# Kernel tuning notes

Measured on AMD Instinct MI355X. Metric: run time of the kernel, lower is better.

## Reference

```python
import jax, jax.numpy as jnp
import numpy as np

K_DEPTH = 3
JAC_A = 1.0  # alpha (Jacobi a)
JAC_B = 1.0  # beta  (Jacobi b)


def jacobi_filter(sig, gammas):
    """Polynomial graph filter g(sigma) = sum_k gamma_k * P_k^{(a,b)}(sigma),
    Jacobi recurrence applied elementwise (Sigma is diagonal spectrum), domain [-1,1],
    fixed inner scalings (fixI=True => alphas=1)."""
    a, b = JAC_A, JAC_B
    xs = [jnp.ones_like(sig)]
    # L = 1
    coef1 = (a - b) / 2.0
    coef2 = (a + b + 2.0) / 2.0
    xs.append(coef1 * xs[0] + coef2 * sig * xs[0])
    for L in range(2, K_DEPTH + 1):
        cl = 2.0 * L * (L + a + b) * (2 * L - 2 + a + b)
        c1 = (2 * L + a + b - 1) * (2 * L + a + b) * (2 * L + a + b - 2)
        c2 = (2 * L + a + b - 1) * (a * a - b * b)
        c3 = 2.0 * (L - 1 + a) * (L - 1 + b) * (2 * L + a + b)
        xs.append((c1 / cl) * sig * xs[-1] - (c2 / cl) * xs[-1] - (c3 / cl) * xs[-2])
    basis = jnp.stack(xs, axis=0)  # [K+1, B, H, L, d]
    return jnp.einsum('k,kbhld->bhld', gammas, basis)


def setup_inputs() -> dict:
    key = jax.random.key(0)
    ks = jax.random.split(key, 7)
    B, L, Ha, Hs, d = 4, 2048, 4, 4, 64
    mk = lambda k, H: jax.random.normal(k, (B, L, H, d), dtype=jnp.float32)
    return {
        'U': mk(ks[0], Ha),
        'Sigma': mk(ks[1], Ha),
        'V': mk(ks[2], Ha),
        'values': mk(ks[3], Ha),
        'queries_softmax': mk(ks[4], Hs),
        'keys_softmax': mk(ks[5], Hs),
        'values_softmax': mk(ks[6], Hs),
        'gammas': jnp.ones((K_DEPTH + 1,), dtype=jnp.float32),
    }


def reference(U, Sigma, V, values, queries_softmax, keys_softmax, values_softmax, gammas):
    d_k = U.shape[-1]
    # ---- AGF (SVD) heads ----
    Uh = jax.nn.softmax(jnp.transpose(U, (0, 2, 1, 3)), axis=-1)        # [B,H,L,d]
    Vt = jax.nn.softmax(jnp.transpose(V, (0, 2, 3, 1)), axis=-1)        # [B,H,d,L]
    vals = jnp.transpose(values, (0, 2, 1, 3))                           # [B,H,L,d]
    sig = jax.nn.sigmoid(jnp.transpose(Sigma, (0, 2, 1, 3)))             # [B,H,L,d]
    gf = jacobi_filter(sig, gammas)                                       # [B,H,L,d]
    kv = jnp.einsum('bhdl,bhle->bhde', Vt, vals)                          # [B,H,d,d]
    out_agf = jnp.einsum('bhld,bhde->bhle', Uh * gf, kv)                  # [B,H,L,d]
    out_agf = jnp.transpose(out_agf, (0, 2, 1, 3))                        # [B,L,H,d]
    # ---- orthogonality loss ----
    eye = jnp.eye(d_k, dtype=Uh.dtype)
    sym_u = jnp.einsum('bhld,bhle->bhde', Uh, Uh) - eye
    sym_v = jnp.einsum('bhdl,bhel->bhde', Vt, Vt) - eye
    ortho_loss = jnp.mean(jnp.abs(sym_u), axis=(1, 2, 3)) + jnp.mean(jnp.abs(sym_v), axis=(1, 2, 3))
    # ---- softmax (flash) heads ----
    q = jnp.transpose(queries_softmax, (0, 2, 1, 3))
    k = jnp.transpose(keys_softmax, (0, 2, 1, 3))
    v = jnp.transpose(values_softmax, (0, 2, 1, 3))
    scores = jnp.einsum('bhld,bhsd->bhls', q, k) / jnp.sqrt(jnp.asarray(d_k, q.dtype))
    attn = jax.nn.softmax(scores, axis=-1)
    out_sm = jnp.einsum('bhls,bhsd->bhld', attn, v)
    out_sm = jnp.transpose(out_sm, (0, 2, 1, 3))                          # [B,L,H,d]
    out = jnp.concatenate([out_agf, out_sm], axis=2)                      # [B,L,2H,d]
    return out, ortho_loss
```

## Files before the change

kernel.cpp:

```cpp
#include <hip/hip_runtime.h>
#include <hip/hip_bf16.h>

#define BB 4
#define SEQ 2048
#define NH 4
#define D 64
#define NPAIR 16
#define HOUT 8
#define LOSS_BASE ((size_t)BB * SEQ * HOUT * D)

#define N_PART   (4 * 16 * 3 * 4096)
#define OFF_SPART N_PART
#define N_SPART  (16 * 32 * 64)
#define OFF_LPART (OFF_SPART + N_SPART)
#define N_LPART  (2 * 16 * 2048)
#define OFF_F32_END (OFF_LPART + N_LPART)
#define USZ ((size_t)16 * 2048 * 64)

typedef __attribute__((ext_vector_type(8))) short bf16x8;
typedef __attribute__((ext_vector_type(4))) float f32x4;
typedef __attribute__((ext_vector_type(8))) unsigned short us8;
typedef __attribute__((ext_vector_type(4))) unsigned short us4;

__device__ __forceinline__ unsigned short f2bf(float x) {
    union { float f; unsigned u; } v; v.f = x;
    unsigned r = v.u + 0x7fffu + ((v.u >> 16) & 1u);
    return (unsigned short)(r >> 16);
}
__device__ __forceinline__ float bf2f(unsigned short u) {
    union { unsigned u; float f; } v; v.u = ((unsigned)u) << 16; return v.f;
}
__device__ __forceinline__ void load16(const float* p, float* v) {
    const float4* q = (const float4*)p;
    float4 a = q[0], b = q[1], c = q[2], d = q[3];
    v[0]=a.x; v[1]=a.y; v[2]=a.z; v[3]=a.w;
    v[4]=b.x; v[5]=b.y; v[6]=b.z; v[7]=b.w;
    v[8]=c.x; v[9]=c.y; v[10]=c.z; v[11]=c.w;
    v[12]=d.x; v[13]=d.y; v[14]=d.z; v[15]=d.w;
}
__device__ __forceinline__ void wr_bf16x16(unsigned short* dst, const float* v) {
    us8 w0, w1;
#pragma unroll
    for (int i = 0; i < 8; i++) { w0[i] = f2bf(v[i]); w1[i] = f2bf(v[8 + i]); }
    *(us8*)dst = w0; *(us8*)(dst + 8) = w1;
}

__global__ __launch_bounds__(256) void prep(const float* __restrict__ U, const float* __restrict__ Sg,
                                            const float* __restrict__ Vagf, const float* __restrict__ vals,
                                            const float* __restrict__ Ksm, const float* __restrict__ Vsm,
                                            const float* __restrict__ gam,
                                            float* __restrict__ ws, unsigned short* __restrict__ usb,
                                            float* __restrict__ out) {
    int lt = blockIdx.x, p = blockIdx.y, stage = blockIdx.z;
    int b = p >> 2, h = p & 3;
    int tid = threadIdx.x;
    int r = tid >> 2;
    int c0 = (tid & 3) * 16;
    __shared__ float T[64][68];
    unsigned short* Khi   = usb;
    unsigned short* VbfT  = usb + USZ;
    unsigned short* UhT   = usb + 2 * USZ;
    unsigned short* EhiT  = usb + 3 * USZ;
    unsigned short* valsT = usb + 4 * USZ;
    unsigned short* Ughi  = usb + 5 * USZ;
    unsigned short* Uglo  = usb + 6 * USZ;
    float* Spart = ws + OFF_SPART;

    const size_t gbase = ((size_t)(b * SEQ + lt * 64 + r) * NH + h) * D + c0;
    const size_t nbase = ((size_t)(p * SEQ + lt * 64 + r)) * 64 + c0;
    const size_t tbase = ((size_t)p * 64 + r) * 2048 + lt * 64 + c0;
    float v[16], e[16];

    if (stage == 0) {
        load16(U + gbase, v);
        float mx = v[0];
#pragma unroll
        for (int k = 1; k < 16; k++) mx = fmaxf(mx, v[k]);
        mx = fmaxf(mx, __shfl_xor(mx, 1));
        mx = fmaxf(mx, __shfl_xor(mx, 2));
        float sm = 0.0f;
#pragma unroll
        for (int k = 0; k < 16; k++) { v[k] = __expf(v[k] - mx); sm += v[k]; }
        sm += __shfl_xor(sm, 1);
        sm += __shfl_xor(sm, 2);
        float inv = 1.0f / sm;
#pragma unroll
        for (int k = 0; k < 16; k++) { v[k] *= inv; T[r][c0 + k] = v[k]; }
        float sg[16];
        load16(Sg + gbase, sg);
        float g0 = gam[0], g1 = gam[1], g2 = gam[2], g3 = gam[3];
        us8 h0, h1, l0, l1;
#pragma unroll
        for (int k = 0; k < 16; k++) {
            float sig = 1.0f / (1.0f + __expf(-sg[k]));
            float x1 = 2.0f * sig;
            float x2 = 1.875f * sig * x1 - 0.75f;
            float x3 = 1.8666666666666667f * sig * x2 - 0.8f * x1;
            float ug = v[k] * (g0 + g1 * x1 + g2 * x2 + g3 * x3);
            unsigned short hh = f2bf(ug);
            unsigned short ll = f2bf(ug - bf2f(hh));
            if (k < 8) { h0[k] = hh; l0[k] = ll; } else { h1[k - 8] = hh; l1[k - 8] = ll; }
        }
        *(us8*)(Ughi + nbase) = h0; *(us8*)(Ughi + nbase + 8) = h1;
        *(us8*)(Uglo + nbase) = l0; *(us8*)(Uglo + nbase + 8) = l1;
        __syncthreads();
#pragma unroll
        for (int k = 0; k < 16; k++) e[k] = T[c0 + k][r];
        wr_bf16x16(UhT + tbase, e);
    } else if (stage == 1) {
        load16(Vagf + gbase, v);
#pragma unroll
        for (int k = 0; k < 16; k++) T[r][c0 + k] = __expf(v[k]);
        __syncthreads();
        float ssum = 0.0f;
#pragma unroll
        for (int k = 0; k < 16; k++) { e[k] = T[c0 + k][r]; ssum += e[k]; }
        ssum += __shfl_xor(ssum, 1);
        ssum += __shfl_xor(ssum, 2);
        if ((tid & 3) == 0) Spart[(p * 32 + lt) * 64 + r] = ssum;
        wr_bf16x16(EhiT + tbase, e);
    } else if (stage == 2) {
        load16(vals + gbase, v);
#pragma unroll
        for (int k = 0; k < 16; k++) T[r][c0 + k] = v[k];
        __syncthreads();
#pragma unroll
        for (int k = 0; k < 16; k++) e[k] = T[c0 + k][r];
        wr_bf16x16(valsT + tbase, e);
    } else if (stage == 3) {
        load16(Vsm + gbase, v);
#pragma unroll
        for (int k = 0; k < 16; k++) T[r][c0 + k] = v[k];
        __syncthreads();
#pragma unroll
        for (int k = 0; k < 16; k++) e[k] = T[c0 + k][r];
        wr_bf16x16(VbfT + tbase, e);
    } else {
        load16(Ksm + gbase, v);
        wr_bf16x16(Khi + nbase, v);
        if (lt == 0 && p == 0 && tid < BB) out[LOSS_BASE + tid] = 0.0f;
    }
}

#define PSTR 72

__global__ __launch_bounds__(256, 2) void mid(const unsigned short* __restrict__ usb,
                                              const float* __restrict__ Q,
                                              float* __restrict__ part,
                                              unsigned short* __restrict__ OpartUS,
                                              float* __restrict__ lpart) {
    __shared__ __align__(16) unsigned char smem[36864];
    const int bid = blockIdx.x;
    const int tid = threadIdx.x;
    const int w = tid >> 6, lane = tid & 63, lm = lane & 15, quad = lane >> 4;

    if (bid >= 64) {
        int fb = bid - 64;
        int qt2 = fb & 15, p = (fb >> 4) & 15, half = fb >> 8;
        int b = p >> 2, h = p & 3;
        const unsigned short* Khi  = usb;
        const unsigned short* VbfT = usb + USZ;
        unsigned short* Kl = (unsigned short*)smem;
        unsigned short* Vl = Kl + 64 * PSTR;
        unsigned short* Ph = Vl + 64 * PSTR;
        const int srow = tid >> 2, sseg = (tid & 3) * 16;

        bf16x8 qhi[2][2], qlo[2][2];
#pragma unroll
        for (int q = 0; q < 2; q++) {
            int row = qt2 * 128 + q * 64 + w * 16 + lm;
            const float* qp = Q + ((size_t)(b * SEQ + row) * NH + h) * D + quad * 8;
#pragma unroll
            for (int ks = 0; ks < 2; ks++) {
                float qq[8];
                float4 a0 = *(const float4*)(qp + ks * 32);
                float4 a1 = *(const float4*)(qp + ks * 32 + 4);
                qq[0]=a0.x; qq[1]=a0.y; qq[2]=a0.z; qq[3]=a0.w;
                qq[4]=a1.x; qq[5]=a1.y; qq[6]=a1.z; qq[7]=a1.w;
#pragma unroll
                for (int j = 0; j < 8; j++) {
                    float xs = qq[j] * 0.125f;
                    unsigned short hi = f2bf(xs);
                    qhi[q][ks][j] = (short)hi;
                    qlo[q][ks][j] = (short)f2bf(xs - bf2f(hi));
                }
            }
        }

        float rsum[2] = {0.f, 0.f};
        f32x4 o[2][4];
#pragma unroll
        for (int q = 0; q < 2; q++)
#pragma unroll
            for (int t = 0; t < 4; t++) o[q][t] = (f32x4){0.f, 0.f, 0.f, 0.f};

        for (int kt = 0; kt < 16; ++kt) {
            __syncthreads();
            {
                size_t kb = ((size_t)(p * SEQ + half * 1024 + kt * 64 + srow)) * 64 + sseg;
                us8 k0 = *(const us8*)(Khi + kb);
                us8 k1 = *(const us8*)(Khi + kb + 8);
                size_t vb = ((size_t)p * 64 + srow) * 2048 + half * 1024 + kt * 64 + sseg;
                us8 v0 = *(const us8*)(VbfT + vb);
                us8 v1 = *(const us8*)(VbfT + vb + 8);
                *(us8*)&Kl[srow * PSTR + sseg] = k0; *(us8*)&Kl[srow * PSTR + sseg + 8] = k1;
                *(us8*)&Vl[srow * PSTR + sseg] = v0; *(us8*)&Vl[srow * PSTR + sseg + 8] = v1;
            }
            __syncthreads();

            bf16x8 kfr[4][2], vfr[4][2];
#pragma unroll
            for (int t = 0; t < 4; t++)
#pragma unroll
                for (int ks = 0; ks < 2; ks++) {
                    kfr[t][ks] = *(const bf16x8*)&Kl[(t * 16 + lm) * PSTR + ks * 32 + quad * 8];
                    vfr[t][ks] = *(const bf16x8*)&Vl[(t * 16 + lm) * PSTR + ks * 32 + quad * 8];
                }

#pragma unroll
            for (int q = 0; q < 2; q++) {
                unsigned short* Phq = Ph + (size_t)(w * 2 + q) * 16 * PSTR;
                f32x4 s[4];
#pragma unroll
                for (int t = 0; t < 4; t++) s[t] = (f32x4){0.f, 0.f, 0.f, 0.f};
#pragma unroll
                for (int t = 0; t < 4; t++)
#pragma unroll
                    for (int ks = 0; ks < 2; ks++) {
                        s[t] = __builtin_amdgcn_mfma_f32_16x16x32_bf16(kfr[t][ks], qhi[q][ks], s[t], 0, 0, 0);
                        s[t] = __builtin_amdgcn_mfma_f32_16x16x32_bf16(kfr[t][ks], qlo[q][ks], s[t], 0, 0, 0);
                    }
#pragma unroll
                for (int t = 0; t < 4; t++) {
                    float e0 = __expf(s[t][0]);
                    float e1 = __expf(s[t][1]);
                    float e2 = __expf(s[t][2]);
                    float e3 = __expf(s[t][3]);
                    rsum[q] += (e0 + e1) + (e2 + e3);
                    us4 pk;
                    pk[0] = f2bf(e0); pk[1] = f2bf(e1); pk[2] = f2bf(e2); pk[3] = f2bf(e3);
                    *(us4*)&Phq[lm * PSTR + t * 16 + quad * 4] = pk;
                }
                bf16x8 pf0 = *(const bf16x8*)&Phq[lm * PSTR + quad * 8];
                bf16x8 pf1 = *(const bf16x8*)&Phq[lm * PSTR + 32 + quad * 8];
#pragma unroll
                for (int dt = 0; dt < 4; dt++) {
                    o[q][dt] = __builtin_amdgcn_mfma_f32_16x16x32_bf16(vfr[dt][0], pf0, o[q][dt], 0, 0, 0);
                    o[q][dt] = __builtin_amdgcn_mfma_f32_16x16x32_bf16(vfr[dt][1], pf1, o[q][dt], 0, 0, 0);
                }
            }
        }

#pragma unroll
        for (int q = 0; q < 2; q++) {
            float rs = rsum[q];
            rs += __shfl_xor(rs, 16);
            rs += __shfl_xor(rs, 32);
            int qrow = qt2 * 128 + q * 64 + w * 16 + lm;
            size_t ob = ((size_t)(half * 16 + p) * SEQ + qrow) * 64;
#pragma unroll
            for (int dt = 0; dt < 4; dt++) {
                us4 pk;
#pragma unroll
                for (int r = 0; r < 4; r++) pk[r] = f2bf(o[q][dt][r]);
                *(us4*)(OpartUS + ob + dt * 16 + quad * 4) = pk;
            }
            if (quad == 0) lpart[(size_t)(half * 16 + p) * SEQ + qrow] = rs;
        }
    } else {
        int split = bid >> 4, p = bid & 15;
        const unsigned short* UhT   = usb + 2 * USZ;
        const unsigned short* EhiT  = usb + 3 * USZ;
        const unsigned short* valsT = usb + 4 * USZ;
        unsigned short* Ut = (unsigned short*)smem;
        unsigned short* Eh = Ut + 64 * 40;
        unsigned short* Vt = Eh + 64 * 40;
        f32x4 su[4], sv[4], kv[4];
#pragma unroll
        for (int i = 0; i < 4; i++) { su[i] = (f32x4){0,0,0,0}; sv[i] = (f32x4){0,0,0,0}; kv[i] = (f32x4){0,0,0,0}; }
        int srow = tid >> 2;
        int sseg = (tid & 3) * 8;

        for (int step = 0; step < 16; ++step) {
            int l0 = split * 512 + step * 32;
            __syncthreads();
            size_t gb = ((size_t)p * 64 + srow) * 2048 + l0 + sseg;
            *(us8*)&Ut[srow * 40 + sseg] = *(const us8*)(UhT + gb);
            *(us8*)&Eh[srow * 40 + sseg] = *(const us8*)(EhiT + gb);
            *(us8*)&Vt[srow * 40 + sseg] = *(const us8*)(valsT + gb);
            __syncthreads();
            int ao = (w * 16 + lm) * 40 + quad * 8;
            bf16x8 au  = *(const bf16x8*)&Ut[ao];
            bf16x8 aeh = *(const bf16x8*)&Eh[ao];
#pragma unroll
            for (int nt = 0; nt < 4; nt++) {
                int bo = (nt * 16 + lm) * 40 + quad * 8;
                bf16x8 bu  = *(const bf16x8*)&Ut[bo];
                bf16x8 beh = *(const bf16x8*)&Eh[bo];
                bf16x8 bv  = *(const bf16x8*)&Vt[bo];
                su[nt] = __builtin_amdgcn_mfma_f32_16x16x32_bf16(au,  bu,  su[nt], 0, 0, 0);
                sv[nt] = __builtin_amdgcn_mfma_f32_16x16x32_bf16(aeh, beh, sv[nt], 0, 0, 0);
                kv[nt] = __builtin_amdgcn_mfma_f32_16x16x32_bf16(aeh, bv,  kv[nt], 0, 0, 0);
            }
        }
        float* dst = part + (size_t)(split * 16 + p) * 3 * 4096;
#pragma unroll
        for (int nt = 0; nt < 4; nt++)
#pragma unroll
            for (int reg = 0; reg < 4; reg++) {
                int off = (w * 16 + quad * 4 + reg) * 64 + nt * 16 + lm;
                dst[off] = su[nt][reg];
                dst[4096 + off] = sv[nt][reg];
                dst[8192 + off] = kv[nt][reg];
            }
    }
}

__global__ __launch_bounds__(256) void post(const float* __restrict__ part, const float* __restrict__ Spart,
                                            const unsigned short* __restrict__ usb,
                                            const unsigned short* __restrict__ OpartUS,
                                            const float* __restrict__ lpart, float* __restrict__ out) {
    const int bid = blockIdx.x;
    const int tid = threadIdx.x;
    if (bid < 2048) {
        int idx = bid * 256 + tid;
        int p = idx >> 15;
        int rem = idx & 32767;
        int l = rem >> 4, dq = rem & 15;
        int b = p >> 2, h = p & 3;
        us4 a = *(const us4*)(OpartUS + ((size_t)p * SEQ + l) * 64 + dq * 4);
        us4 c = *(const us4*)(OpartUS + ((size_t)(16 + p) * SEQ + l) * 64 + dq * 4);
        float inv = 1.0f / (lpart[(size_t)p * SEQ + l] + lpart[(size_t)(16 + p) * SEQ + l]);
        f32x4 res;
#pragma unroll
        for (int r = 0; r < 4; r++) res[r] = (bf2f(a[r]) + bf2f(c[r])) * inv;
        *(f32x4*)(out + ((size_t)(b * SEQ + l) * HOUT + 4 + h) * D + dq * 4) = res;
        return;
    }
    const int w = tid >> 6, lane = tid & 63, lm = lane & 15, quad = lane >> 4;
    int j = bid - 2048;
    int p = (j < 512) ? (j >> 5) : (j - 512);
    __shared__ float cis[64];
    __shared__ float red[4][64];
    __shared__ __align__(16) unsigned short KVh[64 * PSTR];
    __shared__ __align__(16) unsigned short KVl[64 * PSTR];
    {
        int d = tid & 63, grp = tid >> 6;
        float s = 0.0f;
#pragma unroll
        for (int i = 0; i < 8; i++) s += Spart[(p * 32 + grp * 8 + i) * 64 + d];
        red[grp][d] = s;
        __syncthreads();
        if (tid < 64) cis[tid] = 1.0f / (red[0][tid] + red[1][tid] + red[2][tid] + red[3][tid]);
        __syncthreads();
    }
    if (j >= 512) {
        float s = 0.0f;
        for (int idx = tid; idx < 8192; idx += 256) {
            int g = idx >> 12, i = idx & 4095;
            float v = 0.0f;
#pragma unroll
            for (int sp = 0; sp < 4; sp++) v += part[((size_t)(sp * 16 + p) * 3 + g) * 4096 + i];
            if (g) v *= cis[i >> 6] * cis[i & 63];
            float dg = ((i >> 6) == (i & 63)) ? 1.0f : 0.0f;
            s += fabsf(v - dg);
        }
#pragma unroll
        for (int o = 32; o > 0; o >>= 1) s += __shfl_xor(s, o);
        if ((tid & 63) == 0) red[0][(tid >> 6) * 2] = s;
        __syncthreads();
        if (tid == 0)
            atomicAdd(&out[LOSS_BASE + (p >> 2)],
                      (red[0][0] + red[0][2] + red[0][4] + red[0][6]) * (1.0f / 16384.0f));
        return;
    }
    int lt = j & 31;
    int b = p >> 2, h = p & 3;
    const unsigned short* Ughi = usb + 5 * USZ;
    const unsigned short* Uglo = usb + 6 * USZ;
    for (int idx = tid; idx < 4096; idx += 256) {
        int d = idx >> 6, e = idx & 63;
        float v = 0.0f;
#pragma unroll
        for (int sp = 0; sp < 4; sp++) v += part[((size_t)(sp * 16 + p) * 3 + 2) * 4096 + idx];
        v *= cis[d];
        unsigned short hh = f2bf(v);
        KVh[e * PSTR + d] = hh;
        KVl[e * PSTR + d] = f2bf(v - bf2f(hh));
    }
    __syncthreads();
    size_t ub = ((size_t)(p * SEQ + lt * 64 + w * 16 + lm)) * 64 + quad * 8;
    bf16x8 ah[2], al[2];
#pragma unroll
    for (int ks = 0; ks < 2; ks++) {
        ah[ks] = *(const bf16x8*)(Ughi + ub + ks * 32);
        al[ks] = *(const bf16x8*)(Uglo + ub + ks * 32);
    }
    f32x4 acc[4];
#pragma unroll
    for (int nt = 0; nt < 4; nt++) acc[nt] = (f32x4){0.f, 0.f, 0.f, 0.f};
#pragma unroll
    for (int nt = 0; nt < 4; nt++)
#pragma unroll
        for (int ks = 0; ks < 2; ks++) {
            bf16x8 bh = *(const bf16x8*)&KVh[(nt * 16 + lm) * PSTR + ks * 32 + quad * 8];
            bf16x8 bl = *(const bf16x8*)&KVl[(nt * 16 + lm) * PSTR + ks * 32 + quad * 8];
            acc[nt] = __builtin_amdgcn_mfma_f32_16x16x32_bf16(ah[ks], bh, acc[nt], 0, 0, 0);
            acc[nt] = __builtin_amdgcn_mfma_f32_16x16x32_bf16(al[ks], bh, acc[nt], 0, 0, 0);
            acc[nt] = __builtin_amdgcn_mfma_f32_16x16x32_bf16(ah[ks], bl, acc[nt], 0, 0, 0);
        }
#pragma unroll
    for (int nt = 0; nt < 4; nt++)
#pragma unroll
        for (int reg = 0; reg < 4; reg++)
            out[((size_t)(b * SEQ + lt * 64 + w * 16 + quad * 4 + reg) * HOUT + h) * D + nt * 16 + lm] =
                acc[nt][reg];
}

extern "C" void kernel_launch(void* const* d_in, const int* in_sizes, int n_in,
                              void* d_out, int out_size, void* d_ws, size_t ws_size,
                              hipStream_t stream) {
    (void)in_sizes; (void)n_in; (void)out_size; (void)ws_size;
    const float* U    = (const float*)d_in[0];
    const float* Sg   = (const float*)d_in[1];
    const float* V    = (const float*)d_in[2];
    const float* vals = (const float*)d_in[3];
    const float* Qs   = (const float*)d_in[4];
    const float* Ks   = (const float*)d_in[5];
    const float* Vv   = (const float*)d_in[6];
    const float* gam  = (const float*)d_in[7];
    float* out = (float*)d_out;

    float* ws = (float*)d_ws;
    float* part  = ws;
    float* Spart = ws + OFF_SPART;
    float* lpart = ws + OFF_LPART;
    unsigned short* usb = (unsigned short*)(ws + OFF_F32_END);
    unsigned short* OpartUS = usb + 7 * USZ;

    prep<<<dim3(32, 16, 5), 256, 0, stream>>>(U, Sg, V, vals, Ks, Vv, gam, ws, usb, out);
    mid<<<576, 256, 0, stream>>>(usb, Qs, part, OpartUS, lpart);
    post<<<2576, 256, 0, stream>>>(part, Spart, usb, OpartUS, lpart, out);
}
```

Before: 167.0 us.

## Fuse three kernels into one cooperative persistent kernel with grid syncs

Merges prep, mid and post into one cooperative kernel of 576 blocks that uses grid-wide syncs between phases, with a three-launch fallback if the cooperative launch fails. The prep phase now handles all five inputs per block, and most intermediates are stored in natural layout instead of transposed. The gram phase transposes tiles into shared memory itself, and the post phase loops over slices to cover the old 2576-block grid. The aim is to cut launch gaps and transposition cost, at the price of grid-sync overhead and less parallelism per phase.

```diff
diff --git a/kernel.cpp b/kernel.cpp
--- a/kernel.cpp
+++ b/kernel.cpp
@@ -1,11 +1,13 @@
 #include <hip/hip_runtime.h>
 #include <hip/hip_bf16.h>
+#include <hip/hip_cooperative_groups.h>
+
+namespace cg = cooperative_groups;
 
 #define BB 4
 #define SEQ 2048
 #define NH 4
 #define D 64
-#define NPAIR 16
 #define HOUT 8
 #define LOSS_BASE ((size_t)BB * SEQ * HOUT * D)
 
@@ -16,11 +18,23 @@
 #define N_LPART  (2 * 16 * 2048)
 #define OFF_F32_END (OFF_LPART + N_LPART)
 #define USZ ((size_t)16 * 2048 * 64)
+#define PSTR 72
+#define NBLK 576
+#define SMEM_BYTES 36864
 
 typedef __attribute__((ext_vector_type(8))) short bf16x8;
 typedef __attribute__((ext_vector_type(4))) float f32x4;
 typedef __attribute__((ext_vector_type(8))) unsigned short us8;
 typedef __attribute__((ext_vector_type(4))) unsigned short us4;
+
+struct Args {
+    const float *U, *Sg, *Vagf, *vals, *Ksm, *Vsm, *gam, *Q;
+    float *ws, *out;
+};
+struct WSP {
+    float *part, *Spart, *lpart;
+    unsigned short *Khi, *VbfT, *Uhn, *Ehn, *valn, *Ughi, *Uglo, *OpartUS;
+};
 
 __device__ __forceinline__ unsigned short f2bf(float x) {
     union { float f; unsigned u; } v; v.f = x;
@@ -44,51 +58,47 @@
     for (int i = 0; i < 8; i++) { w0[i] = f2bf(v[i]); w1[i] = f2bf(v[8 + i]); }
     *(us8*)dst = w0; *(us8*)(dst + 8) = w1;
 }
-
-__global__ __launch_bounds__(256) void prep(const float* __restrict__ U, const float* __restrict__ Sg,
-                                            const float* __restrict__ Vagf, const float* __restrict__ vals,
-                                            const float* __restrict__ Ksm, const float* __restrict__ Vsm,
-                                            const float* __restrict__ gam,
-                                            float* __restrict__ ws, unsigned short* __restrict__ usb,
-                                            float* __restrict__ out) {
-    int lt = blockIdx.x, p = blockIdx.y, stage = blockIdx.z;
+__device__ __forceinline__ WSP mkws(float* ws) {
+    WSP w;
+    w.part = ws; w.Spart = ws + OFF_SPART; w.lpart = ws + OFF_LPART;
+    unsigned short* usb = (unsigned short*)(ws + OFF_F32_END);
+    w.Khi = usb; w.VbfT = usb + USZ; w.Uhn = usb + 2 * USZ; w.Ehn = usb + 3 * USZ;
+    w.valn = usb + 4 * USZ; w.Ughi = usb + 5 * USZ; w.Uglo = usb + 6 * USZ;
+    w.OpartUS = usb + 7 * USZ;
+    return w;
+}
+
+__device__ void phase_prep(int bid, int tid, unsigned char* smem, const Args& a, const WSP& wsp) {
+    int lt = bid & 31, p = bid >> 5;
     int b = p >> 2, h = p & 3;
-    int tid = threadIdx.x;
     int r = tid >> 2;
     int c0 = (tid & 3) * 16;
-    __shared__ float T[64][68];
-    unsigned short* Khi   = usb;
-    unsigned short* VbfT  = usb + USZ;
-    unsigned short* UhT   = usb + 2 * USZ;
-    unsigned short* EhiT  = usb + 3 * USZ;
-    unsigned short* valsT = usb + 4 * USZ;
-    unsigned short* Ughi  = usb + 5 * USZ;
-    unsigned short* Uglo  = usb + 6 * USZ;
-    float* Spart = ws + OFF_SPART;
-
+    float (*T)[68] = (float(*)[68])smem;
+    float* redp = (float*)(smem + 17408);
     const size_t gbase = ((size_t)(b * SEQ + lt * 64 + r) * NH + h) * D + c0;
     const size_t nbase = ((size_t)(p * SEQ + lt * 64 + r)) * 64 + c0;
     const size_t tbase = ((size_t)p * 64 + r) * 2048 + lt * 64 + c0;
     float v[16], e[16];
 
-    if (stage == 0) {
-        load16(U + gbase, v);
-        float mx = v[0];
-#pragma unroll
-        for (int k = 1; k < 16; k++) mx = fmaxf(mx, v[k]);
-        mx = fmaxf(mx, __shfl_xor(mx, 1));
-        mx = fmaxf(mx, __shfl_xor(mx, 2));
-        float sm = 0.0f;
-#pragma unroll
-        for (int k = 0; k < 16; k++) { v[k] = __expf(v[k] - mx); sm += v[k]; }
-        sm += __shfl_xor(sm, 1);
-        sm += __shfl_xor(sm, 2);
-        float inv = 1.0f / sm;
-#pragma unroll
-        for (int k = 0; k < 16; k++) { v[k] *= inv; T[r][c0 + k] = v[k]; }
+    load16(a.U + gbase, v);
+    float mx = v[0];
+#pragma unroll
+    for (int k = 1; k < 16; k++) mx = fmaxf(mx, v[k]);
+    mx = fmaxf(mx, __shfl_xor(mx, 1));
+    mx = fmaxf(mx, __shfl_xor(mx, 2));
+    float sm = 0.0f;
+#pragma unroll
+    for (int k = 0; k < 16; k++) { v[k] = __expf(v[k] - mx); sm += v[k]; }
+    sm += __shfl_xor(sm, 1);
+    sm += __shfl_xor(sm, 2);
+    float inv = 1.0f / sm;
+#pragma unroll
+    for (int k = 0; k < 16; k++) v[k] *= inv;
+    wr_bf16x16(wsp.Uhn + nbase, v);
+    {
         float sg[16];
-        load16(Sg + gbase, sg);
-        float g0 = gam[0], g1 = gam[1], g2 = gam[2], g3 = gam[3];
+        load16(a.Sg + gbase, sg);
+        float g0 = a.gam[0], g1 = a.gam[1], g2 = a.gam[2], g3 = a.gam[3];
         us8 h0, h1, l0, l1;
 #pragma unroll
         for (int k = 0; k < 16; k++) {
@@ -101,200 +111,200 @@
             unsigned short ll = f2bf(ug - bf2f(hh));
             if (k < 8) { h0[k] = hh; l0[k] = ll; } else { h1[k - 8] = hh; l1[k - 8] = ll; }
         }
-        *(us8*)(Ughi + nbase) = h0; *(us8*)(Ughi + nbase + 8) = h1;
-        *(us8*)(Uglo + nbase) = l0; *(us8*)(Uglo + nbase + 8) = l1;
-        __syncthreads();
-#pragma unroll
-        for (int k = 0; k < 16; k++) e[k] = T[c0 + k][r];
-        wr_bf16x16(UhT + tbase, e);
-    } else if (stage == 1) {
-        load16(Vagf + gbase, v);
-#pragma unroll
-        for (int k = 0; k < 16; k++) T[r][c0 + k] = __expf(v[k]);
-        __syncthreads();
-        float ssum = 0.0f;
-#pragma unroll
-        for (int k = 0; k < 16; k++) { e[k] = T[c0 + k][r]; ssum += e[k]; }
-        ssum += __shfl_xor(ssum, 1);
-        ssum += __shfl_xor(ssum, 2);
-        if ((tid & 3) == 0) Spart[(p * 32 + lt) * 64 + r] = ssum;
-        wr_bf16x16(EhiT + tbase, e);
-    } else if (stage == 2) {
-        load16(vals + gbase, v);
-#pragma unroll
-        for (int k = 0; k < 16; k++) T[r][c0 + k] = v[k];
-        __syncthreads();
-#pragma unroll
-        for (int k = 0; k < 16; k++) e[k] = T[c0 + k][r];
-        wr_bf16x16(valsT + tbase, e);
-    } else if (stage == 3) {
-        load16(Vsm + gbase, v);
-#pragma unroll
-        for (int k = 0; k < 16; k++) T[r][c0 + k] = v[k];
-        __syncthreads();
-#pragma unroll
-        for (int k = 0; k < 16; k++) e[k] = T[c0 + k][r];
-        wr_bf16x16(VbfT + tbase, e);
-    } else {
-        load16(Ksm + gbase, v);
-        wr_bf16x16(Khi + nbase, v);
-        if (lt == 0 && p == 0 && tid < BB) out[LOSS_BASE + tid] = 0.0f;
-    }
-}
-
-#define PSTR 72
-
-__global__ __launch_bounds__(256, 2) void mid(const unsigned short* __restrict__ usb,
-                                              const float* __restrict__ Q,
-                                              float* __restrict__ part,
-                                              unsigned short* __restrict__ OpartUS,
-                                              float* __restrict__ lpart) {
-    __shared__ __align__(16) unsigned char smem[36864];
-    const int bid = blockIdx.x;
-    const int tid = threadIdx.x;
+        *(us8*)(wsp.Ughi + nbase) = h0; *(us8*)(wsp.Ughi + nbase + 8) = h1;
+        *(us8*)(wsp.Uglo + nbase) = l0; *(us8*)(wsp.Uglo + nbase + 8) = l1;
+    }
+
+    load16(a.Vagf + gbase, v);
+#pragma unroll
+    for (int k = 0; k < 16; k++) { v[k] = __expf(v[k]); T[r][c0 + k] = v[k]; }
+    wr_bf16x16(wsp.Ehn + nbase, v);
+    __syncthreads();
+    {
+        int d = tid & 63, grp = tid >> 6;
+        float s = 0.0f;
+#pragma unroll
+        for (int i = 0; i < 16; i++) s += T[grp * 16 + i][d];
+        redp[grp * 64 + d] = s;
+        __syncthreads();
+        if (tid < 64)
+            wsp.Spart[(p * 32 + lt) * 64 + tid] =
+                redp[tid] + redp[64 + tid] + redp[128 + tid] + redp[192 + tid];
+    }
+
+    load16(a.vals + gbase, v);
+    wr_bf16x16(wsp.valn + nbase, v);
+
+    load16(a.Vsm + gbase, v);
+    __syncthreads();
+#pragma unroll
+    for (int k = 0; k < 16; k++) T[r][c0 + k] = v[k];
+    __syncthreads();
+#pragma unroll
+    for (int k = 0; k < 16; k++) e[k] = T[c0 + k][r];
+    wr_bf16x16(wsp.VbfT + tbase, e);
+
+    load16(a.Ksm + gbase, v);
+    wr_bf16x16(wsp.Khi + nbase, v);
+
+    if (bid == 0 && tid < BB) a.out[LOSS_BASE + tid] = 0.0f;
+}
+
+__device__ void phase_flash(int fb, int tid, unsigned char* smem, const Args& a, const WSP& wsp) {
     const int w = tid >> 6, lane = tid & 63, lm = lane & 15, quad = lane >> 4;
-
-    if (bid >= 64) {
-        int fb = bid - 64;
-        int qt2 = fb & 15, p = (fb >> 4) & 15, half = fb >> 8;
-        int b = p >> 2, h = p & 3;
-        const unsigned short* Khi  = usb;
-        const unsigned short* VbfT = usb + USZ;
-        unsigned short* Kl = (unsigned short*)smem;
-        unsigned short* Vl = Kl + 64 * PSTR;
-        unsigned short* Ph = Vl + 64 * PSTR;
-        const int srow = tid >> 2, sseg = (tid & 3) * 16;
-
-        bf16x8 qhi[2][2], qlo[2][2];
+    int qt2 = fb & 15, p = (fb >> 4) & 15, half = fb >> 8;
+    int b = p >> 2, h = p & 3;
+    unsigned short* Kl = (unsigned short*)smem;
+    unsigned short* Vl = Kl + 64 * PSTR;
+    unsigned short* Ph = Vl + 64 * PSTR;
+    const int srow = tid >> 2, sseg = (tid & 3) * 16;
+
+    bf16x8 qhi[2][2], qlo[2][2];
+#pragma unroll
+    for (int q = 0; q < 2; q++) {
+        int row = qt2 * 128 + q * 64 + w * 16 + lm;
+        const float* qp = a.Q + ((size_t)(b * SEQ + row) * NH + h) * D + quad * 8;
+#pragma unroll
+        for (int ks = 0; ks < 2; ks++) {
+            float qq[8];
+            float4 a0 = *(const float4*)(qp + ks * 32);
+            float4 a1 = *(const float4*)(qp + ks * 32 + 4);
+            qq[0]=a0.x; qq[1]=a0.y; qq[2]=a0.z; qq[3]=a0.w;
+            qq[4]=a1.x; qq[5]=a1.y; qq[6]=a1.z; qq[7]=a1.w;
+#pragma unroll
+            for (int j = 0; j < 8; j++) {
+                float xs = qq[j] * 0.125f;
+                unsigned short hi = f2bf(xs);
+                qhi[q][ks][j] = (short)hi;
+                qlo[q][ks][j] = (short)f2bf(xs - bf2f(hi));
+            }
+        }
+    }
+
+    float rsum[2] = {0.f, 0.f};
+    f32x4 o[2][4];
+#pragma unroll
+    for (int q = 0; q < 2; q++)
+#pragma unroll
+        for (int t = 0; t < 4; t++) o[q][t] = (f32x4){0.f, 0.f, 0.f, 0.f};
+
+    for (int kt = 0; kt < 16; ++kt) {
+        __syncthreads();
+        {
+            size_t kb = ((size_t)(p * SEQ + half * 1024 + kt * 64 + srow)) * 64 + sseg;
+            us8 k0 = *(const us8*)(wsp.Khi + kb);
+            us8 k1 = *(const us8*)(wsp.Khi + kb + 8);
+            size_t vb = ((size_t)p * 64 + srow) * 2048 + half * 1024 + kt * 64 + sseg;
+            us8 v0 = *(const us8*)(wsp.VbfT + vb);
+            us8 v1 = *(const us8*)(wsp.VbfT + vb + 8);
+            *(us8*)&Kl[srow * PSTR + sseg] = k0; *(us8*)&Kl[srow * PSTR + sseg + 8] = k1;
+            *(us8*)&Vl[srow * PSTR + sseg] = v0; *(us8*)&Vl[srow * PSTR + sseg + 8] = v1;
+        }
+        __syncthreads();
+
+        bf16x8 kfr[4][2], vfr[4][2];
+#pragma unroll
+        for (int t = 0; t < 4; t++)
+#pragma unroll
+            for (int ks = 0; ks < 2; ks++) {
+                kfr[t][ks] = *(const bf16x8*)&Kl[(t * 16 + lm) * PSTR + ks * 32 + quad * 8];
+                vfr[t][ks] = *(const bf16x8*)&Vl[(t * 16 + lm) * PSTR + ks * 32 + quad * 8];
+            }
+
 #pragma unroll
         for (int q = 0; q < 2; q++) {
-            int row = qt2 * 128 + q * 64 + w * 16 + lm;
-            const float* qp = Q + ((size_t)(b * SEQ + row) * NH + h) * D + quad * 8;
-#pragma unroll
-            for (int ks = 0; ks < 2; ks++) {
-                float qq[8];
-                float4 a0 = *(const float4*)(qp + ks * 32);
-                float4 a1 = *(const float4*)(qp + ks * 32 + 4);
-                qq[0]=a0.x; qq[1]=a0.y; qq[2]=a0.z; qq[3]=a0.w;
-                qq[4]=a1.x; qq[5]=a1.y; qq[6]=a1.z; qq[7]=a1.w;
-#pragma unroll
-                for (int j = 0; j < 8; j++) {
-                    float xs = qq[j] * 0.125f;
-                    unsigned short hi = f2bf(xs);
-                    qhi[q][ks][j] = (short)hi;
-                    qlo[q][ks][j] = (short)f2bf(xs - bf2f(hi));
+            unsigned short* Phq = Ph + (size_t)(w * 2 + q) * 16 * PSTR;
+            f32x4 s[4];
+#pragma unroll
+            for (int t = 0; t < 4; t++) s[t] = (f32x4){0.f, 0.f, 0.f, 0.f};
+#pragma unroll
+            for (int t = 0; t < 4; t++)
+#pragma unroll
+                for (int ks = 0; ks < 2; ks++) {
+                    s[t] = __builtin_amdgcn_mfma_f32_16x16x32_bf16(kfr[t][ks], qhi[q][ks], s[t], 0, 0, 0);
+                    s[t] = __builtin_amdgcn_mfma_f32_16x16x32_bf16(kfr[t][ks], qlo[q][ks], s[t], 0, 0, 0);
                 }
-            }
-        }
-
-        float rsum[2] = {0.f, 0.f};
-        f32x4 o[2][4];
-#pragma unroll
-        for (int q = 0; q < 2; q++)
-#pragma unroll
-            for (int t = 0; t < 4; t++) o[q][t] = (f32x4){0.f, 0.f, 0.f, 0.f};
-
-        for (int kt = 0; kt < 16; ++kt) {
-            __syncthreads();
-            {
-                size_t kb = ((size_t)(p * SEQ + half * 1024 + kt * 64 + srow)) * 64 + sseg;
-                us8 k0 = *(const us8*)(Khi + kb);
-                us8 k1 = *(const us8*)(Khi + kb + 8);
-                size_t vb = ((size_t)p * 64 + srow) * 2048 + half * 1024 + kt * 64 + sseg;
-                us8 v0 = *(const us8*)(VbfT + vb);
-                us8 v1 = *(const us8*)(VbfT + vb + 8);
-                *(us8*)&Kl[srow * PSTR + sseg] = k0; *(us8*)&Kl[srow * PSTR + sseg + 8] = k1;
-                *(us8*)&Vl[srow * PSTR + sseg] = v0; *(us8*)&Vl[srow * PSTR + sseg + 8] = v1;
-            }
-            __syncthreads();
-
-            bf16x8 kfr[4][2], vfr[4][2];
-#pragma unroll
-            for (int t = 0; t < 4; t++)
-#pragma unroll
-                for (int ks = 0; ks < 2; ks++) {
-                    kfr[t][ks] = *(const bf16x8*)&Kl[(t * 16 + lm) * PSTR + ks * 32 + quad * 8];
-                    vfr[t][ks] = *(const bf16x8*)&Vl[(t * 16 + lm) * PSTR + ks * 32 + quad * 8];
+#pragma unroll
+            for (int t = 0; t < 4; t++) {
+                float e0 = __expf(s[t][0]);
+                float e1 = __expf(s[t][1]);
+                float e2 = __expf(s[t][2]);
+                float e3 = __expf(s[t][3]);
+                rsum[q] += (e0 + e1) + (e2 + e3);
+                us4 pk;
+                pk[0] = f2bf(e0); pk[1] = f2bf(e1); pk[2] = f2bf(e2); pk[3] = f2bf(e3);
+                *(us4*)&Phq[lm * PSTR + t * 16 + quad * 4] = pk;
+            }
+            bf16x8 pf0 = *(const bf16x8*)&Phq[lm * PSTR + quad * 8];
+            bf16x8 pf1 = *(const bf16x8*)&Phq[lm * PSTR + 32 + quad * 8];
+#pragma unroll
+            for (int dt = 0; dt < 4; dt++) {
+                o[q][dt] = __builtin_amdgcn_mfma_f32_16x16x32_bf16(vfr[dt][0], pf0, o[q][dt], 0, 0, 0);
+                o[q][dt] = __builtin_amdgcn_mfma_f32_16x16x32_bf16(vfr[dt][1], pf1, o[q][dt], 0, 0, 0);
+            }
+        }
+    }
+
+#pragma unroll
+    for (int q = 0; q < 2; q++) {
+        float rs = rsum[q];
+        rs += __shfl_xor(rs, 16);
+        rs += __shfl_xor(rs, 32);
+        int qrow = qt2 * 128 + q * 64 + w * 16 + lm;
+        size_t ob = ((size_t)(half * 16 + p) * SEQ + qrow) * 64;
+#pragma unroll
+        for (int dt = 0; dt < 4; dt++) {
+            us4 pk;
+#pragma unroll
+            for (int r = 0; r < 4; r++) pk[r] = f2bf(o[q][dt][r]);
+            *(us4*)(wsp.OpartUS + ob + dt * 16 + quad * 4) = pk;
+        }
+        if (quad == 0) wsp.lpart[(size_t)(half * 16 + p) * SEQ + qrow] = rs;
+    }
+}
+
+__device__ void phase_gram(int g, int tid, unsigned char* smem, const Args& a, const WSP& wsp) {
+    const int w = tid >> 6, lane = tid & 63, lm = lane & 15, quad = lane >> 4;
+    int split = g >> 4, p = g & 15;
+    unsigned short* Ut = (unsigned short*)smem;
+    unsigned short* Eh = Ut + 64 * PSTR;
+    unsigned short* Vt = Eh + 64 * PSTR;
+    f32x4 su[4], sv[4], kv[4];
+#pragma unroll
+    for (int i = 0; i < 4; i++) { su[i] = (f32x4){0,0,0,0}; sv[i] = (f32x4){0,0,0,0}; kv[i] = (f32x4){0,0,0,0}; }
+    int r0 = (tid & 15) * 4;
+    int c0t = (tid >> 4) * 4;
+
+    for (int step = 0; step < 8; ++step) {
+        int l0 = split * 512 + step * 64;
+        __syncthreads();
+        {
+            const unsigned short* srcs[3] = {wsp.Uhn, wsp.Ehn, wsp.valn};
+            unsigned short* dsts[3] = {Ut, Eh, Vt};
+#pragma unroll
+            for (int ai = 0; ai < 3; ai++) {
+                us4 rowv[4];
+#pragma unroll
+                for (int i = 0; i < 4; i++)
+                    rowv[i] = *(const us4*)(srcs[ai] + ((size_t)p * 2048 + l0 + r0 + i) * 64 + c0t);
+#pragma unroll
+                for (int c = 0; c < 4; c++) {
+                    us4 col;
+#pragma unroll
+                    for (int i = 0; i < 4; i++) col[i] = rowv[i][c];
+                    *(us4*)&dsts[ai][(c0t + c) * PSTR + r0] = col;
                 }
-
-#pragma unroll
-            for (int q = 0; q < 2; q++) {
-                unsigned short* Phq = Ph + (size_t)(w * 2 + q) * 16 * PSTR;
-                f32x4 s[4];
-#pragma unroll
-                for (int t = 0; t < 4; t++) s[t] = (f32x4){0.f, 0.f, 0.f, 0.f};
-#pragma unroll
-                for (int t = 0; t < 4; t++)
-#pragma unroll
-                    for (int ks = 0; ks < 2; ks++) {
-                        s[t] = __builtin_amdgcn_mfma_f32_16x16x32_bf16(kfr[t][ks], qhi[q][ks], s[t], 0, 0, 0);
-                        s[t] = __builtin_amdgcn_mfma_f32_16x16x32_bf16(kfr[t][ks], qlo[q][ks], s[t], 0, 0, 0);
-                    }
-#pragma unroll
-                for (int t = 0; t < 4; t++) {
-                    float e0 = __expf(s[t][0]);
-                    float e1 = __expf(s[t][1]);
-                    float e2 = __expf(s[t][2]);
-                    float e3 = __expf(s[t][3]);
-                    rsum[q] += (e0 + e1) + (e2 + e3);
-                    us4 pk;
-                    pk[0] = f2bf(e0); pk[1] = f2bf(e1); pk[2] = f2bf(e2); pk[3] = f2bf(e3);
-                    *(us4*)&Phq[lm * PSTR + t * 16 + quad * 4] = pk;
-                }
-                bf16x8 pf0 = *(const bf16x8*)&Phq[lm * PSTR + quad * 8];
-                bf16x8 pf1 = *(const bf16x8*)&Phq[lm * PSTR + 32 + quad * 8];
-#pragma unroll
-                for (int dt = 0; dt < 4; dt++) {
-                    o[q][dt] = __builtin_amdgcn_mfma_f32_16x16x32_bf16(vfr[dt][0], pf0, o[q][dt], 0, 0, 0);
-                    o[q][dt] = __builtin_amdgcn_mfma_f32_16x16x32_bf16(vfr[dt][1], pf1, o[q][dt], 0, 0, 0);
-                }
-            }
-        }
-
-#pragma unroll
-        for (int q = 0; q < 2; q++) {
-            float rs = rsum[q];
-            rs += __shfl_xor(rs, 16);
-            rs += __shfl_xor(rs, 32);
-            int qrow = qt2 * 128 + q * 64 + w * 16 + lm;
-            size_t ob = ((size_t)(half * 16 + p) * SEQ + qrow) * 64;
-#pragma unroll
-            for (int dt = 0; dt < 4; dt++) {
-                us4 pk;
-#pragma unroll
-                for (int r = 0; r < 4; r++) pk[r] = f2bf(o[q][dt][r]);
-                *(us4*)(OpartUS + ob + dt * 16 + quad * 4) = pk;
-            }
-            if (quad == 0) lpart[(size_t)(half * 16 + p) * SEQ + qrow] = rs;
-        }
-    } else {
-        int split = bid >> 4, p = bid & 15;
-        const unsigned short* UhT   = usb + 2 * USZ;
-        const unsigned short* EhiT  = usb + 3 * USZ;
-        const unsigned short* valsT = usb + 4 * USZ;
-        unsigned short* Ut = (unsigned short*)smem;
-        unsigned short* Eh = Ut + 64 * 40;
-        unsigned short* Vt = Eh + 64 * 40;
-        f32x4 su[4], sv[4], kv[4];
-#pragma unroll
-        for (int i = 0; i < 4; i++) { su[i] = (f32x4){0,0,0,0}; sv[i] = (f32x4){0,0,0,0}; kv[i] = (f32x4){0,0,0,0}; }
-        int srow = tid >> 2;
-        int sseg = (tid & 3) * 8;
-
-        for (int step = 0; step < 16; ++step) {
-            int l0 = split * 512 + step * 32;
-            __syncthreads();
-            size_t gb = ((size_t)p * 64 + srow) * 2048 + l0 + sseg;
-            *(us8*)&Ut[srow * 40 + sseg] = *(const us8*)(UhT + gb);
-            *(us8*)&Eh[srow * 40 + sseg] = *(const us8*)(EhiT + gb);
-            *(us8*)&Vt[srow * 40 + sseg] = *(const us8*)(valsT + gb);
-            __syncthreads();
-            int ao = (w * 16 + lm) * 40 + quad * 8;
+            }
+        }
+        __syncthreads();
+#pragma unroll
+        for (int ks = 0; ks < 2; ks++) {
+            int ao = (w * 16 + lm) * PSTR + ks * 32 + quad * 8;
             bf16x8 au  = *(const bf16x8*)&Ut[ao];
             bf16x8 aeh = *(const bf16x8*)&Eh[ao];
 #pragma unroll
             for (int nt = 0; nt < 4; nt++) {
-                int bo = (nt * 16 + lm) * 40 + quad * 8;
+                int bo = (nt * 16 + lm) * PSTR + ks * 32 + quad * 8;
                 bf16x8 bu  = *(const bf16x8*)&Ut[bo];
                 bf16x8 beh = *(const bf16x8*)&Eh[bo];
                 bf16x8 bv  = *(const bf16x8*)&Vt[bo];
@@ -303,86 +313,83 @@
                 kv[nt] = __builtin_amdgcn_mfma_f32_16x16x32_bf16(aeh, bv,  kv[nt], 0, 0, 0);
             }
         }
-        float* dst = part + (size_t)(split * 16 + p) * 3 * 4096;
-#pragma unroll
-        for (int nt = 0; nt < 4; nt++)
-#pragma unroll
-            for (int reg = 0; reg < 4; reg++) {
-                int off = (w * 16 + quad * 4 + reg) * 64 + nt * 16 + lm;
-                dst[off] = su[nt][reg];
-                dst[4096 + off] = sv[nt][reg];
-                dst[8192 + off] = kv[nt][reg];
-            }
-    }
-}
-
-__global__ __launch_bounds__(256) void post(const float* __restrict__ part, const float* __restrict__ Spart,
-                                            const unsigned short* __restrict__ usb,
-                                            const unsigned short* __restrict__ OpartUS,
-                                            const float* __restrict__ lpart, float* __restrict__ out) {
-    const int bid = blockIdx.x;
-    const int tid = threadIdx.x;
-    if (bid < 2048) {
-        int idx = bid * 256 + tid;
-        int p = idx >> 15;
-        int rem = idx & 32767;
-        int l = rem >> 4, dq = rem & 15;
-        int b = p >> 2, h = p & 3;
-        us4 a = *(const us4*)(OpartUS + ((size_t)p * SEQ + l) * 64 + dq * 4);
-        us4 c = *(const us4*)(OpartUS + ((size_t)(16 + p) * SEQ + l) * 64 + dq * 4);
-        float inv = 1.0f / (lpart[(size_t)p * SEQ + l] + lpart[(size_t)(16 + p) * SEQ + l]);
-        f32x4 res;
-#pragma unroll
-        for (int r = 0; r < 4; r++) res[r] = (bf2f(a[r]) + bf2f(c[r])) * inv;
-        *(f32x4*)(out + ((size_t)(b * SEQ + l) * HOUT + 4 + h) * D + dq * 4) = res;
-        return;
-    }
+    }
+    float* dst = wsp.part + (size_t)(split * 16 + p) * 3 * 4096;
+#pragma unroll
+    for (int nt = 0; nt < 4; nt++)
+#pragma unroll
+        for (int reg = 0; reg < 4; reg++) {
+            int off = (w * 16 + quad * 4 + reg) * 64 + nt * 16 + lm;
+            dst[off] = su[nt][reg];
+            dst[4096 + off] = sv[nt][reg];
+            dst[8192 + off] = kv[nt][reg];
+        }
+}
+
+__device__ void phase_post(int bid, int tid, unsigned char* smem, const Args& a, const WSP& wsp) {
+#pragma unroll
+    for (int k = 0; k < 4; k++) {
+        int slice = bid + k * NBLK;
+        if (slice < 2048) {
+            int idx = slice * 256 + tid;
+            int p = idx >> 15;
+            int rem = idx & 32767;
+            int l = rem >> 4, dq = rem & 15;
+            int b = p >> 2, h = p & 3;
+            us4 x = *(const us4*)(wsp.OpartUS + ((size_t)p * SEQ + l) * 64 + dq * 4);
+            us4 y = *(const us4*)(wsp.OpartUS + ((size_t)(16 + p) * SEQ + l) * 64 + dq * 4);
+            float inv = 1.0f / (wsp.lpart[(size_t)p * SEQ + l] + wsp.lpart[(size_t)(16 + p) * SEQ + l]);
+            f32x4 res;
+#pragma unroll
+            for (int r = 0; r < 4; r++) res[r] = (bf2f(x[r]) + bf2f(y[r])) * inv;
+            *(f32x4*)(a.out + ((size_t)(b * SEQ + l) * HOUT + 4 + h) * D + dq * 4) = res;
+        }
+    }
+    if (bid >= 528) return;
     const int w = tid >> 6, lane = tid & 63, lm = lane & 15, quad = lane >> 4;
-    int j = bid - 2048;
-    int p = (j < 512) ? (j >> 5) : (j - 512);
-    __shared__ float cis[64];
-    __shared__ float red[4][64];
-    __shared__ __align__(16) unsigned short KVh[64 * PSTR];
-    __shared__ __align__(16) unsigned short KVl[64 * PSTR];
+    int p = (bid < 512) ? (bid >> 5) : (bid - 512);
+    float* cis = (float*)smem;
+    float* redp = (float*)(smem + 256);
+    unsigned short* KVh = (unsigned short*)(smem + 1280);
+    unsigned short* KVl = (unsigned short*)(smem + 1280 + 64 * PSTR * 2);
     {
         int d = tid & 63, grp = tid >> 6;
         float s = 0.0f;
 #pragma unroll
-        for (int i = 0; i < 8; i++) s += Spart[(p * 32 + grp * 8 + i) * 64 + d];
-        red[grp][d] = s;
-        __syncthreads();
-        if (tid < 64) cis[tid] = 1.0f / (red[0][tid] + red[1][tid] + red[2][tid] + red[3][tid]);
-        __syncthreads();
-    }
-    if (j >= 512) {
+        for (int i = 0; i < 8; i++) s += wsp.Spart[(p * 32 + grp * 8 + i) * 64 + d];
+        redp[grp * 64 + d] = s;
+        __syncthreads();
+        if (tid < 64) cis[tid] = 1.0f / (redp[tid] + redp[64 + tid] + redp[128 + tid] + redp[192 + tid]);
+        __syncthreads();
+    }
+    if (bid >= 512) {
         float s = 0.0f;
         for (int idx = tid; idx < 8192; idx += 256) {
             int g = idx >> 12, i = idx & 4095;
             float v = 0.0f;
 #pragma unroll
-            for (int sp = 0; sp < 4; sp++) v += part[((size_t)(sp * 16 + p) * 3 + g) * 4096 + i];
+            for (int sp = 0; sp < 4; sp++) v += wsp.part[((size_t)(sp * 16 + p) * 3 + g) * 4096 + i];
             if (g) v *= cis[i >> 6] * cis[i & 63];
             float dg = ((i >> 6) == (i & 63)) ? 1.0f : 0.0f;
             s += fabsf(v - dg);
         }
 #pragma unroll
         for (int o = 32; o > 0; o >>= 1) s += __shfl_xor(s, o);
-        if ((tid & 63) == 0) red[0][(tid >> 6) * 2] = s;
+        __syncthreads();
+        if ((tid & 63) == 0) redp[tid >> 6] = s;
         __syncthreads();
         if (tid == 0)
-            atomicAdd(&out[LOSS_BASE + (p >> 2)],
-                      (red[0][0] + red[0][2] + red[0][4] + red[0][6]) * (1.0f / 16384.0f));
+            atomicAdd(&a.out[LOSS_BASE + (p >> 2)],
+                      (redp[0] + redp[1] + redp[2] + redp[3]) * (1.0f / 16384.0f));
         return;
     }
-    int lt = j & 31;
+    int lt = bid & 31;
     int b = p >> 2, h = p & 3;
-    const unsigned short* Ughi = usb + 5 * USZ;
-    const unsigned short* Uglo = usb + 6 * USZ;
     for (int idx = tid; idx < 4096; idx += 256) {
         int d = idx >> 6, e = idx & 63;
         float v = 0.0f;
 #pragma unroll
-        for (int sp = 0; sp < 4; sp++) v += part[((size_t)(sp * 16 + p) * 3 + 2) * 4096 + idx];
+        for (int sp = 0; sp < 4; sp++) v += wsp.part[((size_t)(sp * 16 + p) * 3 + 2) * 4096 + idx];
         v *= cis[d];
         unsigned short hh = f2bf(v);
         KVh[e * PSTR + d] = hh;
@@ -393,8 +400,8 @@
     bf16x8 ah[2], al[2];
 #pragma unroll
     for (int ks = 0; ks < 2; ks++) {
-        ah[ks] = *(const bf16x8*)(Ughi + ub + ks * 32);
-        al[ks] = *(const bf16x8*)(Uglo + ub + ks * 32);
+        ah[ks] = *(const bf16x8*)(wsp.Ughi + ub + ks * 32);
+        al[ks] = *(const bf16x8*)(wsp.Uglo + ub + ks * 32);
     }
     f32x4 acc[4];
 #pragma unroll
@@ -413,32 +420,61 @@
     for (int nt = 0; nt < 4; nt++)
 #pragma unroll
         for (int reg = 0; reg < 4; reg++)
-            out[((size_t)(b * SEQ + lt * 64 + w * 16 + quad * 4 + reg) * HOUT + h) * D + nt * 16 + lm] =
+            a.out[((size_t)(b * SEQ + lt * 64 + w * 16 + quad * 4 + reg) * HOUT + h) * D + nt * 16 + lm] =
                 acc[nt][reg];
+}
+
+__global__ __launch_bounds__(256, 3) void fused(Args a) {
+    __shared__ __align__(16) unsigned char smem[SMEM_BYTES];
+    const int bid = blockIdx.x, tid = threadIdx.x;
+    WSP wsp = mkws(a.ws);
+    if (bid < 512) phase_prep(bid, tid, smem, a, wsp);
+    cg::this_grid().sync();
+    if (bid < 512) phase_flash(bid, tid, smem, a, wsp);
+    else phase_gram(bid - 512, tid, smem, a, wsp);
+    cg::this_grid().sync();
+    phase_post(bid, tid, smem, a, wsp);
+}
+
+__global__ __launch_bounds__(256, 3) void prep_k(Args a) {
+    __shared__ __align__(16) unsigned char smem[SMEM_BYTES];
+    WSP wsp = mkws(a.ws);
+    phase_prep(blockIdx.x, threadIdx.x, smem, a, wsp);
+}
+__global__ __launch_bounds__(256, 3) void mid_k(Args a) {
+    __shared__ __align__(16) unsigned char smem[SMEM_BYTES];
+    WSP wsp = mkws(a.ws);
+    if (blockIdx.x < 512) phase_flash(blockIdx.x, threadIdx.x, smem, a, wsp);
+    else phase_gram(blockIdx.x - 512, threadIdx.x, smem, a, wsp);
+}
+__global__ __launch_bounds__(256, 3) void post_k(Args a) {
+    __shared__ __align__(16) unsigned char smem[SMEM_BYTES];
+    WSP wsp = mkws(a.ws);
+    phase_post(blockIdx.x, threadIdx.x, smem, a, wsp);
 }
 
 extern "C" void kernel_launch(void* const* d_in, const int* in_sizes, int n_in,
                               void* d_out, int out_size, void* d_ws, size_t ws_size,
                               hipStream_t stream) {
     (void)in_sizes; (void)n_in; (void)out_size; (void)ws_size;
-    const float* U    = (const float*)d_in[0];
-    const float* Sg   = (const float*)d_in[1];
-    const float* V    = (const float*)d_in[2];
-    const float* vals = (const float*)d_in[3];
-    const float* Qs   = (const float*)d_in[4];
-    const float* Ks   = (const float*)d_in[5];
-    const float* Vv   = (const float*)d_in[6];
-    const float* gam  = (const float*)d_in[7];
-    float* out = (float*)d_out;
-
-    float* ws = (float*)d_ws;
-    float* part  = ws;
-    float* Spart = ws + OFF_SPART;
-    float* lpart = ws + OFF_LPART;
-    unsigned short* usb = (unsigned short*)(ws + OFF_F32_END);
-    unsigned short* OpartUS = usb + 7 * USZ;
-
-    prep<<<dim3(32, 16, 5), 256, 0, stream>>>(U, Sg, V, vals, Ks, Vv, gam, ws, usb, out);
-    mid<<<576, 256, 0, stream>>>(usb, Qs, part, OpartUS, lpart);
-    post<<<2576, 256, 0, stream>>>(part, Spart, usb, OpartUS, lpart, out);
-}
+    Args a;
+    a.U    = (const float*)d_in[0];
+    a.Sg   = (const float*)d_in[1];
+    a.Vagf = (const float*)d_in[2];
+    a.vals = (const float*)d_in[3];
+    a.Q    = (const float*)d_in[4];
+    a.Ksm  = (const float*)d_in[5];
+    a.Vsm  = (const float*)d_in[6];
+    a.gam  = (const float*)d_in[7];
+    a.ws   = (float*)d_ws;
+    a.out  = (float*)d_out;
+
+    void* kargs[] = {&a};
+    hipError_t err = hipLaunchCooperativeKernel(fused, dim3(NBLK), dim3(256), kargs, 0, stream);
+    if (err != hipSuccess) {
+        (void)hipGetLastError();
+        prep_k<<<512, 256, 0, stream>>>(a);
+        mid_k<<<NBLK, 256, 0, stream>>>(a);
+        post_k<<<NBLK, 256, 0, stream>>>(a);
+    }
+}
```

Result: slower. 339.2 us (+103.2%).
